# Performance work log

Hardware: AMD Instinct MI355X
Metric: run time of the kernel (lower is better)

The kernel has to match this reference:

```python
import jax, jax.numpy as jnp
import numpy as np

B, T, C, K, V = 4, 4096, 128, 64, 64
EPS = 1e-5


def layer_norm(x, g, b):
    mu = jnp.mean(x, axis=-1, keepdims=True)
    var = jnp.var(x, axis=-1, keepdims=True)
    return (x - mu) * jax.lax.rsqrt(var + EPS) * g + b


def setup_inputs() -> dict:
    key = jax.random.key(0)
    ks = jax.random.split(key, 8)
    s = 1.0 / np.sqrt(C)
    return {
        "x": jax.random.normal(ks[0], (B, T, C), dtype=jnp.float32),
        "Wq": jax.random.uniform(ks[1], (C, K), jnp.float32, -s, s),
        "bq": jnp.zeros((K,), jnp.float32),
        "Wk": jax.random.uniform(ks[2], (C, K), jnp.float32, -s, s),
        "bk": jnp.zeros((K,), jnp.float32),
        "Wv": jax.random.uniform(ks[3], (C, V), jnp.float32, -s, s),
        "bv": jnp.zeros((V,), jnp.float32),
        "gq": jnp.ones((K,), jnp.float32), "bgq": jnp.zeros((K,), jnp.float32),
        "gk": jnp.ones((K,), jnp.float32), "bgk": jnp.zeros((K,), jnp.float32),
        "gv": jnp.ones((V,), jnp.float32), "bgv": jnp.zeros((V,), jnp.float32),
        "go": jnp.ones((V,), jnp.float32), "bgo": jnp.zeros((V,), jnp.float32),
    }


def reference(x, Wq, bq, Wk, bk, Wv, bv, gq, bgq, gk, bgk, gv, bgv, go, bgo):
    # projections: B x T x {K,K,V}
    q = layer_norm(x @ Wq + bq, gq, bgq)
    k = layer_norm(x @ Wk + bk, gk, bgk)
    v = layer_norm(x @ Wv + bv, gv, bgv)
    sqrt_k = jnp.asarray(np.sqrt(K), x.dtype)
    # full B x T x T causal score matrix (faithful to the original bmm+mask)
    logits = jnp.einsum("btk,bsk->bts", q, k) / sqrt_k
    t = jnp.arange(T)
    causal = t[:, None] >= t[None, :]  # lower-triangular incl. diagonal
    logits = jnp.where(causal[None], logits, -jnp.inf)
    probs = jax.nn.softmax(logits, axis=-1)
    read = jnp.einsum("bts,bsv->btv", probs, v)
    read = layer_norm(read, go, bgo)
    return jnp.concatenate([x, read], axis=2)  # B x T x (C+V)
```

## Files before the change

### kernel.cpp

```cpp
#include <hip/hip_runtime.h>

#define TT 4096

typedef unsigned short u16;
typedef unsigned int u32;

typedef short bf16x8 __attribute__((ext_vector_type(8)));
typedef float f32x4 __attribute__((ext_vector_type(4)));

union U8 {
  uint2 q[2];
  uint4 u4;
  bf16x8 v;
  short s[8];
  u32 w[4];
};

static __device__ __forceinline__ u16 f2bf(float f) {
  union { float f; u32 u; } cv;
  cv.f = f;
  u32 r = cv.u + 0x7FFFu + ((cv.u >> 16) & 1u);
  return (u16)(r >> 16);
}
static __device__ __forceinline__ u32 pk2(float a, float b) {
  return (u32)f2bf(a) | ((u32)f2bf(b) << 16);
}
static __device__ __forceinline__ float bf2f(u16 h) {
  union { u32 u; float f; } cv;
  cv.u = ((u32)h) << 16;
  return cv.f;
}
static __device__ __forceinline__ float exp2a(float x) {
  float r; asm("v_exp_f32 %0, %1" : "=v"(r) : "v"(x)); return r;
}
static __device__ __forceinline__ u32 cvtpk(float lo, float hi) {
  u32 r; asm("v_cvt_pk_bf16_f32 %0, %1, %2" : "=v"(r) : "v"(lo), "v"(hi)); return r;
}

__global__ __launch_bounds__(64)
void wpack(const float* __restrict__ Wq, const float* __restrict__ Wk,
           const float* __restrict__ Wv, u16* __restrict__ wf)
{
  const int g = blockIdx.x;
  const int p = g >> 4, s = (g >> 2) & 3, nt = g & 3;
  const int l = threadIdx.x, lg = l >> 4, l15 = l & 15;
  const float* W = (p == 0) ? Wq : (p == 1) ? Wk : Wv;
  const int n = l15 + 16 * nt;
  U8 o;
#pragma unroll
  for (int j = 0; j < 8; ++j) {
    int k = 32 * s + ((j < 4) ? (4 * lg + j) : (16 + 4 * lg + (j - 4)));
    o.s[j] = (short)f2bf(W[k * 64 + n]);
  }
  *(uint4*)(wf + (size_t)(g * 64 + l) * 8) = o.u4;
}

__global__ __launch_bounds__(256)
void proj_mfma(const float* __restrict__ x, const u16* __restrict__ wf,
               const float* __restrict__ bq, const float* __restrict__ bk,
               const float* __restrict__ bv,
               const float* __restrict__ gq, const float* __restrict__ bgq,
               const float* __restrict__ gk, const float* __restrict__ bgk,
               const float* __restrict__ gv, const float* __restrict__ bgv,
               u16* __restrict__ qo, u16* __restrict__ ko, u16* __restrict__ vto,
               float* __restrict__ out)
{
  __shared__ u16 xs[64 * 128];
  const int bx = blockIdx.x;
  const int xcd = bx & 7, i = bx >> 3;
  const int tile = xcd * 32 + (i & 31);
  const int p = i >> 5;
  const int rowbase = tile * 64;
  const int t = threadIdx.x;

  {
    const int row = t >> 2, seg = t & 3;
    const float4* src = (const float4*)(x + (size_t)(rowbase + row) * 128 + seg * 32);
    float4 f[8];
#pragma unroll
    for (int q = 0; q < 8; ++q) f[q] = src[q];
    if ((p == 0 && seg < 2) || (p == 1 && seg >= 2)) {
      float4* dst = (float4*)(out + (size_t)(rowbase + row) * 192 + seg * 32);
#pragma unroll
      for (int q = 0; q < 8; ++q) dst[q] = f[q];
    }
    const int base = row * 256 + seg * 64;
    const int swz = (row & 7) << 4;
    char* xb = (char*)xs;
#pragma unroll
    for (int q = 0; q < 4; ++q) {
      uint4 u;
      u.x = pk2(f[2 * q].x, f[2 * q].y);
      u.y = pk2(f[2 * q].z, f[2 * q].w);
      u.z = pk2(f[2 * q + 1].x, f[2 * q + 1].y);
      u.w = pk2(f[2 * q + 1].z, f[2 * q + 1].w);
      *(uint4*)(xb + ((base + 16 * q) ^ swz)) = u;
    }
  }

  const int w = t >> 6, l = t & 63, lg = l >> 4, l15 = l & 15;
  U8 bfr[4][4];
  const u16* wp = wf + (size_t)p * (16 * 64 * 8);
#pragma unroll
  for (int s = 0; s < 4; ++s)
#pragma unroll
    for (int nt = 0; nt < 4; ++nt)
      bfr[s][nt].u4 = *(const uint4*)(wp + ((s * 4 + nt) * 64 + l) * 8);

  __syncthreads();

  f32x4 acc[4];
#pragma unroll
  for (int nt = 0; nt < 4; ++nt) acc[nt] = (f32x4){0.f, 0.f, 0.f, 0.f};
  const int abase = (16 * w + l15) * 256;
  const int aswz = (l15 & 7) << 4;
  const char* xb = (const char*)xs;
#pragma unroll
  for (int s = 0; s < 4; ++s) {
    U8 af;
    af.q[0] = *(const uint2*)(xb + ((abase + s * 64 + 8 * lg) ^ aswz));
    af.q[1] = *(const uint2*)(xb + ((abase + s * 64 + 8 * lg + 32) ^ aswz));
#pragma unroll
    for (int nt = 0; nt < 4; ++nt)
      acc[nt] = __builtin_amdgcn_mfma_f32_16x16x32_bf16(af.v, bfr[s][nt].v, acc[nt], 0, 0, 0);
  }

  const float* bb = (p == 0) ? bq : (p == 1) ? bk : bv;
  const float* gg = (p == 0) ? gq : (p == 1) ? gk : gv;
  const float* hh = (p == 0) ? bgq : (p == 1) ? bgk : bgv;
  float bcol[4], gcol[4], hcol[4];
#pragma unroll
  for (int nt = 0; nt < 4; ++nt) {
    int col = l15 + 16 * nt;
    bcol[nt] = bb[col]; gcol[nt] = gg[col]; hcol[nt] = hh[col];
  }
  float vals[4][4];
#pragma unroll
  for (int nt = 0; nt < 4; ++nt)
#pragma unroll
    for (int r = 0; r < 4; ++r) vals[nt][r] = acc[nt][r] + bcol[nt];

  float s1[4], s2[4];
#pragma unroll
  for (int r = 0; r < 4; ++r) {
    s1[r] = vals[0][r] + vals[1][r] + vals[2][r] + vals[3][r];
    s2[r] = vals[0][r] * vals[0][r] + vals[1][r] * vals[1][r]
          + vals[2][r] * vals[2][r] + vals[3][r] * vals[3][r];
#pragma unroll
    for (int d = 1; d < 16; d <<= 1) {
      s1[r] += __shfl_xor(s1[r], d);
      s2[r] += __shfl_xor(s2[r], d);
    }
  }

  if (p < 2) {
    u16* dst = (p == 0) ? qo : ko;
#pragma unroll
    for (int r = 0; r < 4; ++r) {
      float mu = s1[r] * (1.f / 64.f);
      float var = s2[r] * (1.f / 64.f) - mu * mu;
      float rs = rsqrtf(var + 1e-5f);
      int grow = rowbase + 16 * w + 4 * lg + r;
#pragma unroll
      for (int nt = 0; nt < 4; ++nt)
        dst[(size_t)grow * 64 + l15 + 16 * nt] =
            f2bf((vals[nt][r] - mu) * rs * gcol[nt] + hcol[nt]);
    }
  } else {
    const int b = rowbase >> 12;
    const int tl0 = (rowbase & 4095) + 16 * w + 4 * lg;
#pragma unroll
    for (int r = 0; r < 4; ++r) {
      float mu = s1[r] * (1.f / 64.f);
      float var = s2[r] * (1.f / 64.f) - mu * mu;
      float rs = rsqrtf(var + 1e-5f);
#pragma unroll
      for (int nt = 0; nt < 4; ++nt)
        vto[(size_t)(b * 64 + l15 + 16 * nt) * TT + tl0 + r] =
            f2bf((vals[nt][r] - mu) * rs * gcol[nt] + hcol[nt]);
    }
  }
}

__global__ __launch_bounds__(256)
void attn_seg4(const u16* __restrict__ qg, const u16* __restrict__ kg,
               const u16* __restrict__ vtg,
               float* __restrict__ mP, float* __restrict__ lP,
               u16* __restrict__ aP)
{
  __shared__ u16 kl4[4 * 64 * 64];
  __shared__ u16 vl4[4 * 64 * 64];
  const int bx = blockIdx.x;
  const int xcd = bx & 7, b = xcd >> 1, e = xcd & 1;
  const int j = e * 272 + (bx >> 3);
  int Q = 0;
  while (2 * (Q + 1) * (Q + 2) <= j) ++Q;
  const int ip = j - 2 * Q * (Q + 1);
  const int dv = ip / (Q + 1);
  const int q = 4 * Q + dv;
  const int s = ip - dv * (Q + 1);
  const int q0 = q * 64;
  const int it0 = s * 4;
  const int it1 = min(it0 + 4, q + 1);

  const int t = threadIdx.x;
  const int w = t >> 6, l = t & 63;
  const int l15 = l & 15, lg = l >> 4;
  const int swzl = (l15 & 7) << 4;

  const int qrow = q0 + 16 * w + l15;
  const u16* qrp = qg + (size_t)(b * TT + qrow) * 64;
  U8 qf[2];
#pragma unroll
  for (int hh = 0; hh < 2; ++hh) {
    qf[hh].q[0] = *(const uint2*)(qrp + 32 * hh + 4 * lg);
    qf[hh].q[1] = *(const uint2*)(qrp + 32 * hh + 4 * lg + 16);
  }

  {
    const int key = t >> 2, part = t & 3;
    const int sbase = key * 128 + part * 32;
    const int ssw = (key & 7) << 4;
    uint4 kr[4][2], vr[4][2];
#pragma unroll
    for (int tt = 0; tt < 4; ++tt) {
      int tile = it0 + tt; if (tile >= it1) tile = it1 - 1;
      const u16* ks = kg + (size_t)(b * TT + tile * 64 + key) * 64 + part * 16;
      kr[tt][0] = ((const uint4*)ks)[0];
      kr[tt][1] = ((const uint4*)ks)[1];
      const u16* vs = vtg + (size_t)(b * 64 + key) * TT + tile * 64 + part * 16;
      vr[tt][0] = ((const uint4*)vs)[0];
      vr[tt][1] = ((const uint4*)vs)[1];
    }
#pragma unroll
    for (int tt = 0; tt < 4; ++tt) {
      char* kd = (char*)kl4 + tt * 8192;
      char* vd = (char*)vl4 + tt * 8192;
      *(uint4*)(kd + ((sbase + 0) ^ ssw)) = kr[tt][0];
      *(uint4*)(kd + ((sbase + 16) ^ ssw)) = kr[tt][1];
      *(uint4*)(vd + ((sbase + 0) ^ ssw)) = vr[tt][0];
      *(uint4*)(vd + ((sbase + 16) ^ ssw)) = vr[tt][1];
    }
  }
  __syncthreads();

  const float C = 0.18033688011112042f;
  float m_run = -1e30f, l_run = 0.f;
  f32x4 acc[4];
#pragma unroll
  for (int ct = 0; ct < 4; ++ct) acc[ct] = (f32x4){0.f, 0.f, 0.f, 0.f};

  int toff = 0;
  for (int it = it0; it < it1; ++it, toff += 8192) {
    const int kb = it * 64;
    const char* kp = (const char*)kl4 + toff;
    const char* vp = (const char*)vl4 + toff;

    f32x4 st[4];
    __builtin_amdgcn_s_setprio(1);
#pragma unroll
    for (int t4 = 0; t4 < 4; ++t4) {
      const int rbase = (16 * t4 + l15) * 128 + 8 * lg;
      U8 kf0, kf1;
      kf0.q[0] = *(const uint2*)(kp + ((rbase + 0) ^ swzl));
      kf0.q[1] = *(const uint2*)(kp + ((rbase + 32) ^ swzl));
      kf1.q[0] = *(const uint2*)(kp + ((rbase + 64) ^ swzl));
      kf1.q[1] = *(const uint2*)(kp + ((rbase + 96) ^ swzl));
      f32x4 d = {0.f, 0.f, 0.f, 0.f};
      d = __builtin_amdgcn_mfma_f32_16x16x32_bf16(kf0.v, qf[0].v, d, 0, 0, 0);
      d = __builtin_amdgcn_mfma_f32_16x16x32_bf16(kf1.v, qf[1].v, d, 0, 0, 0);
      st[t4] = d;
    }
    __builtin_amdgcn_s_setprio(0);

    float sv[16];
    const bool needmask = (kb + 63 > q0 + 16 * w);
    if (needmask) {
#pragma unroll
      for (int t4 = 0; t4 < 4; ++t4) {
#pragma unroll
        for (int r = 0; r < 4; ++r) {
          float sc = st[t4][r] * C;
          int keyidx = kb + 16 * t4 + 4 * lg + r;
          sv[t4 * 4 + r] = (keyidx > qrow) ? -1e30f : sc;
        }
      }
    } else {
#pragma unroll
      for (int t4 = 0; t4 < 4; ++t4) {
#pragma unroll
        for (int r = 0; r < 4; ++r) sv[t4 * 4 + r] = st[t4][r] * C;
      }
    }
    float mx[8];
#pragma unroll
    for (int i = 0; i < 8; ++i) mx[i] = fmaxf(sv[2 * i], sv[2 * i + 1]);
#pragma unroll
    for (int i = 0; i < 4; ++i) mx[i] = fmaxf(mx[2 * i], mx[2 * i + 1]);
    float mt = fmaxf(fmaxf(mx[0], mx[1]), fmaxf(mx[2], mx[3]));
    mt = fmaxf(mt, __shfl_xor(mt, 16));
    mt = fmaxf(mt, __shfl_xor(mt, 32));

    if (!__all(mt - m_run <= 11.5f)) {
      const float mnew = fmaxf(m_run, mt);
      const float al = exp2a(m_run - mnew);
      l_run *= al;
      float ar[4];
#pragma unroll
      for (int r = 0; r < 4; ++r) ar[r] = __shfl(al, 4 * lg + r);
#pragma unroll
      for (int ct = 0; ct < 4; ++ct) {
#pragma unroll
        for (int r = 0; r < 4; ++r) acc[ct][r] *= ar[r];
      }
      m_run = mnew;
    }
    float p[16];
#pragma unroll
    for (int i = 0; i < 16; ++i) p[i] = exp2a(sv[i] - m_run);
    float sm[8];
#pragma unroll
    for (int i = 0; i < 8; ++i) sm[i] = p[2 * i] + p[2 * i + 1];
#pragma unroll
    for (int i = 0; i < 4; ++i) sm[i] = sm[2 * i] + sm[2 * i + 1];
    float rsum = (sm[0] + sm[1]) + (sm[2] + sm[3]);
    rsum += __shfl_xor(rsum, 16);
    rsum += __shfl_xor(rsum, 32);
    l_run += rsum;

    U8 pa[2];
#pragma unroll
    for (int u = 0; u < 2; ++u) {
#pragma unroll
      for (int k2 = 0; k2 < 4; ++k2)
        pa[u].w[k2] = cvtpk(p[8 * u + 2 * k2], p[8 * u + 2 * k2 + 1]);
    }

    __builtin_amdgcn_s_setprio(1);
#pragma unroll
    for (int ct = 0; ct < 4; ++ct) {
      const int vb = (16 * ct + l15) * 128 + 8 * lg;
#pragma unroll
      for (int u = 0; u < 2; ++u) {
        U8 vf;
        vf.q[0] = *(const uint2*)(vp + ((vb + 64 * u + 0) ^ swzl));
        vf.q[1] = *(const uint2*)(vp + ((vb + 64 * u + 32) ^ swzl));
        acc[ct] = __builtin_amdgcn_mfma_f32_16x16x32_bf16(pa[u].v, vf.v, acc[ct], 0, 0, 0);
      }
    }
    __builtin_amdgcn_s_setprio(0);
  }

  const size_t pbase = (size_t)(b * 544 + j) * 64;
  if (lg == 0) {
    mP[pbase + 16 * w + l15] = m_run;
    lP[pbase + 16 * w + l15] = l_run;
  }
#pragma unroll
  for (int ct = 0; ct < 4; ++ct) {
#pragma unroll
    for (int r = 0; r < 4; ++r) {
      int rin = 16 * w + 4 * lg + r;
      aP[(pbase + rin) * 64 + l15 + 16 * ct] = f2bf(acc[ct][r]);
    }
  }
}

__global__ __launch_bounds__(256)
void attn_merge4(const float* __restrict__ mP, const float* __restrict__ lP,
                 const u16* __restrict__ aP,
                 const float* __restrict__ go, const float* __restrict__ bgo,
                 float* __restrict__ out)
{
  const int t = threadIdx.x;
  const int w = t >> 6, c = t & 63;
  const int row = blockIdx.x * 4 + w;
  const int tid2 = row >> 6, rin = row & 63;
  const int b = tid2 >> 6, q = tid2 & 63;
  const int Q = q >> 2;
  const int base_q = b * 544 + 2 * Q * (Q + 1) + (q & 3) * (Q + 1);
  const int ns = Q + 1;

  float m = -1e30f, L = 0.f, o = 0.f;
  for (int s = 0; s < ns; ++s) {
    const size_t pb = (size_t)(base_q + s) * 64;
    float ms = mP[pb + rin];
    float ls = lP[pb + rin];
    float a = bf2f(aP[(pb + rin) * 64 + c]);
    float mn = fmaxf(m, ms);
    float w0 = exp2a(m - mn), w1 = exp2a(ms - mn);
    L = L * w0 + ls * w1;
    o = o * w0 + a * w1;
    m = mn;
  }
  o /= L;

  float s1 = o, s2 = o * o;
#pragma unroll
  for (int d = 1; d < 64; d <<= 1) {
    s1 += __shfl_xor(s1, d);
    s2 += __shfl_xor(s2, d);
  }
  float mu = s1 * (1.f / 64.f);
  float var = s2 * (1.f / 64.f) - mu * mu;
  float rs = rsqrtf(var + 1e-5f);
  out[(size_t)row * 192 + 128 + c] = (o - mu) * rs * go[c] + bgo[c];
}

__global__ __launch_bounds__(256)
void attn_splitW(const u16* __restrict__ qg, const u16* __restrict__ kg,
                 const u16* __restrict__ vtg,
                 float* __restrict__ mP, float* __restrict__ lP,
                 u16* __restrict__ aP,
                 int Wseg, int maxseg, int halfcnt)
{
  __shared__ u16 kl[64 * 64];
  __shared__ u16 vl[64 * 64];
  const int bx = blockIdx.x;
  const int xcd = bx & 7, b = xcd >> 1, e = xcd & 1;
  const int j = e * halfcnt + (bx >> 3);
  const int Wh = Wseg >> 1;
  int Q = 0;
  while (Wh * (Q + 1) * (Q + 2) <= j) ++Q;
  const int ip = j - Wh * Q * (Q + 1);
  const int dv = ip / (Q + 1);
  const int q = Wseg * Q + dv;
  const int s = ip - dv * (Q + 1);
  const int q0 = q * 64;
  const int tileid = b * 64 + q;
  const int it0 = s * Wseg;
  const int it1 = min(it0 + Wseg, q + 1);

  const int t = threadIdx.x;
  const int w = t >> 6, l = t & 63;
  const int l15 = l & 15, lg = l >> 4;
  const int swzl = (l15 & 7) << 4;

  const int qrow = q0 + 16 * w + l15;
  const u16* qrp = qg + (size_t)(b * TT + qrow) * 64;
  U8 qf[2];
#pragma unroll
  for (int hh = 0; hh < 2; ++hh) {
    qf[hh].q[0] = *(const uint2*)(qrp + 32 * hh + 4 * lg);
    qf[hh].q[1] = *(const uint2*)(qrp + 32 * hh + 4 * lg + 16);
  }

  const int key = t >> 2;
  const int part = t & 3;
  const int sbase = key * 128 + part * 32;
  const int ssw = (key & 7) << 4;
  uint4 kr0, kr1, vr0, vr1;
  {
    const u16* ks = kg + (size_t)(b * TT + it0 * 64 + key) * 64 + part * 16;
    kr0 = ((const uint4*)ks)[0];
    kr1 = ((const uint4*)ks)[1];
    const u16* vs = vtg + (size_t)(b * 64 + key) * TT + it0 * 64 + part * 16;
    vr0 = ((const uint4*)vs)[0];
    vr1 = ((const uint4*)vs)[1];
  }

  float m_run = -1e30f, l_run = 0.f;
  f32x4 acc[4];
#pragma unroll
  for (int ct = 0; ct < 4; ++ct) acc[ct] = (f32x4){0.f, 0.f, 0.f, 0.f};

  for (int it = it0; it < it1; ++it) {
    const int kb = it * 64;
    {
      char* kd = (char*)kl;
      char* vd = (char*)vl;
      *(uint4*)(kd + ((sbase + 0) ^ ssw)) = kr0;
      *(uint4*)(kd + ((sbase + 16) ^ ssw)) = kr1;
      *(uint4*)(vd + ((sbase + 0) ^ ssw)) = vr0;
      *(uint4*)(vd + ((sbase + 16) ^ ssw)) = vr1;
    }
    __syncthreads();
    if (it + 1 < it1) {
      const u16* ks = kg + (size_t)(b * TT + (it + 1) * 64 + key) * 64 + part * 16;
      kr0 = ((const uint4*)ks)[0];
      kr1 = ((const uint4*)ks)[1];
      const u16* vs = vtg + (size_t)(b * 64 + key) * TT + (it + 1) * 64 + part * 16;
      vr0 = ((const uint4*)vs)[0];
      vr1 = ((const uint4*)vs)[1];
    }

    f32x4 st[4];
#pragma unroll
    for (int t4 = 0; t4 < 4; ++t4) {
      const int rbase = (16 * t4 + l15) * 128 + 8 * lg;
      const char* kp = (const char*)kl;
      U8 kf0, kf1;
      kf0.q[0] = *(const uint2*)(kp + ((rbase + 0) ^ swzl));
      kf0.q[1] = *(const uint2*)(kp + ((rbase + 32) ^ swzl));
      kf1.q[0] = *(const uint2*)(kp + ((rbase + 64) ^ swzl));
      kf1.q[1] = *(const uint2*)(kp + ((rbase + 96) ^ swzl));
      f32x4 d = {0.f, 0.f, 0.f, 0.f};
      d = __builtin_amdgcn_mfma_f32_16x16x32_bf16(kf0.v, qf[0].v, d, 0, 0, 0);
      d = __builtin_amdgcn_mfma_f32_16x16x32_bf16(kf1.v, qf[1].v, d, 0, 0, 0);
      st[t4] = d;
    }

    float sv[16];
    const bool needmask = (kb + 63 > q0 + 16 * w);
#pragma unroll
    for (int t4 = 0; t4 < 4; ++t4) {
#pragma unroll
      for (int r = 0; r < 4; ++r) {
        float sc = st[t4][r] * 0.125f;
        if (needmask) {
          int keyidx = kb + 16 * t4 + 4 * lg + r;
          if (keyidx > qrow) sc = -1e30f;
        }
        sv[t4 * 4 + r] = sc;
      }
    }
    float mt = sv[0];
#pragma unroll
    for (int i = 1; i < 16; ++i) mt = fmaxf(mt, sv[i]);
    mt = fmaxf(mt, __shfl_xor(mt, 16));
    mt = fmaxf(mt, __shfl_xor(mt, 32));
    const float mnew = fmaxf(m_run, mt);
    const float al = __expf(m_run - mnew);
    float pv[16];
    float rsum = 0.f;
#pragma unroll
    for (int i = 0; i < 16; ++i) { pv[i] = __expf(sv[i] - mnew); rsum += pv[i]; }
    rsum += __shfl_xor(rsum, 16);
    rsum += __shfl_xor(rsum, 32);
    l_run = l_run * al + rsum;
    m_run = mnew;
    float ar[4];
#pragma unroll
    for (int r = 0; r < 4; ++r) ar[r] = __shfl(al, 4 * lg + r);
#pragma unroll
    for (int ct = 0; ct < 4; ++ct) {
#pragma unroll
      for (int r = 0; r < 4; ++r) acc[ct][r] *= ar[r];
    }
    U8 pa[2];
#pragma unroll
    for (int u = 0; u < 2; ++u) {
#pragma unroll
      for (int i = 0; i < 8; ++i) pa[u].s[i] = (short)f2bf(pv[8 * u + i]);
    }

#pragma unroll
    for (int ct = 0; ct < 4; ++ct) {
      const int vb = (16 * ct + l15) * 128 + 8 * lg;
      const char* vp = (const char*)vl;
#pragma unroll
      for (int u = 0; u < 2; ++u) {
        U8 vf;
        vf.q[0] = *(const uint2*)(vp + ((vb + 64 * u + 0) ^ swzl));
        vf.q[1] = *(const uint2*)(vp + ((vb + 64 * u + 32) ^ swzl));
        acc[ct] = __builtin_amdgcn_mfma_f32_16x16x32_bf16(pa[u].v, vf.v, acc[ct], 0, 0, 0);
      }
    }
    __syncthreads();
  }

  const size_t pbase = (size_t)(tileid * maxseg + s) * 64;
  if (lg == 0) {
    mP[pbase + 16 * w + l15] = m_run;
    lP[pbase + 16 * w + l15] = l_run;
  }
#pragma unroll
  for (int ct = 0; ct < 4; ++ct) {
#pragma unroll
    for (int r = 0; r < 4; ++r) {
      int rin = 16 * w + 4 * lg + r;
      aP[(pbase + rin) * 64 + l15 + 16 * ct] = f2bf(acc[ct][r]);
    }
  }
}

__global__ __launch_bounds__(256)
void attn_mergeW(const float* __restrict__ mP, const float* __restrict__ lP,
                 const u16* __restrict__ aP,
                 const float* __restrict__ go, const float* __restrict__ bgo,
                 float* __restrict__ out, int jshift, int maxseg)
{
  const int t = threadIdx.x;
  const int w = t >> 6, c = t & 63;
  const int row = blockIdx.x * 4 + w;
  const int tid2 = row >> 6, rin = row & 63;
  const int q = tid2 & 63;
  const int ns = (q >> jshift) + 1;

  float m = -1e30f, L = 0.f, o = 0.f;
  for (int s = 0; s < ns; ++s) {
    const size_t pbase = (size_t)(tid2 * maxseg + s) * 64;
    float ms = mP[pbase + rin];
    float ls = lP[pbase + rin];
    float a = bf2f(aP[(pbase + rin) * 64 + c]);
    float mn = fmaxf(m, ms);
    float w0 = __expf(m - mn), w1 = __expf(ms - mn);
    L = L * w0 + ls * w1;
    o = o * w0 + a * w1;
    m = mn;
  }
  o /= L;

  float s1 = o, s2 = o * o;
#pragma unroll
  for (int d = 1; d < 64; d <<= 1) {
    s1 += __shfl_xor(s1, d);
    s2 += __shfl_xor(s2, d);
  }
  float mu = s1 * (1.f / 64.f);
  float var = s2 * (1.f / 64.f) - mu * mu;
  float rs = rsqrtf(var + 1e-5f);
  out[(size_t)row * 192 + 128 + c] = (o - mu) * rs * go[c] + bgo[c];
}

__global__ __launch_bounds__(128)
void attn1(const u16* __restrict__ qg, const u16* __restrict__ kg,
           const u16* __restrict__ vtg,
           const float* __restrict__ go, const float* __restrict__ bgo,
           float* __restrict__ out)
{
  __shared__ u16 kl[64 * 64];
  __shared__ u16 vl[64 * 64];
  const int bx = blockIdx.x;
  const int tt = (bx < 256) ? bx : (767 - bx);
  const int b = tt >> 7;
  const int q0 = (tt & 127) * 32;
  const int tid = threadIdx.x;
  const int w = tid >> 6;
  const int l = tid & 63;
  const int l15 = l & 15;
  const int lg = l >> 4;
  const int swzl = (l15 & 7) << 4;

  const int qrow = q0 + 16 * w + l15;
  const u16* qrp = qg + (size_t)(b * TT + qrow) * 64;
  U8 qf[2];
#pragma unroll
  for (int h = 0; h < 2; ++h) {
    qf[h].q[0] = *(const uint2*)(qrp + 32 * h + 4 * lg);
    qf[h].q[1] = *(const uint2*)(qrp + 32 * h + 4 * lg + 16);
  }

  float m_run = -1e30f, l_run = 0.f;
  f32x4 acc[4];
#pragma unroll
  for (int ct = 0; ct < 4; ++ct) acc[ct] = (f32x4){0.f, 0.f, 0.f, 0.f};

  const int nkv = (q0 >> 6) + 1;
  for (int it = 0; it < nkv; ++it) {
    const int kb = it * 64;
    {
      const int key = tid >> 1;
      const int dh = (tid & 1) * 32;
      const u16* ks = kg + (size_t)(b * TT + kb + key) * 64 + dh;
      uint4 d0 = *(const uint4*)(ks + 0);
      uint4 d1 = *(const uint4*)(ks + 8);
      uint4 d2 = *(const uint4*)(ks + 16);
      uint4 d3 = *(const uint4*)(ks + 24);
      const int base = key * 128 + dh * 2;
      const int sw = (key & 7) << 4;
      char* kd = (char*)kl;
      *(uint4*)(kd + ((base + 0) ^ sw)) = d0;
      *(uint4*)(kd + ((base + 16) ^ sw)) = d1;
      *(uint4*)(kd + ((base + 32) ^ sw)) = d2;
      *(uint4*)(kd + ((base + 48) ^ sw)) = d3;
      const u16* vs = vtg + (size_t)(b * 64 + key) * TT + kb + dh;
      uint4 e0 = *(const uint4*)(vs + 0);
      uint4 e1 = *(const uint4*)(vs + 8);
      uint4 e2 = *(const uint4*)(vs + 16);
      uint4 e3 = *(const uint4*)(vs + 24);
      char* vd = (char*)vl;
      *(uint4*)(vd + ((base + 0) ^ sw)) = e0;
      *(uint4*)(vd + ((base + 16) ^ sw)) = e1;
      *(uint4*)(vd + ((base + 32) ^ sw)) = e2;
      *(uint4*)(vd + ((base + 48) ^ sw)) = e3;
    }
    __syncthreads();

    f32x4 st[4];
#pragma unroll
    for (int t4 = 0; t4 < 4; ++t4) {
      const int rbase = (16 * t4 + l15) * 128 + 8 * lg;
      const char* kp = (const char*)kl;
      U8 kf0, kf1;
      kf0.q[0] = *(const uint2*)(kp + ((rbase + 0) ^ swzl));
      kf0.q[1] = *(const uint2*)(kp + ((rbase + 32) ^ swzl));
      kf1.q[0] = *(const uint2*)(kp + ((rbase + 64) ^ swzl));
      kf1.q[1] = *(const uint2*)(kp + ((rbase + 96) ^ swzl));
      f32x4 d = {0.f, 0.f, 0.f, 0.f};
      d = __builtin_amdgcn_mfma_f32_16x16x32_bf16(kf0.v, qf[0].v, d, 0, 0, 0);
      d = __builtin_amdgcn_mfma_f32_16x16x32_bf16(kf1.v, qf[1].v, d, 0, 0, 0);
      st[t4] = d;
    }

    float sv[16];
    const bool needmask = (kb + 63 > q0 + 16 * w);
#pragma unroll
    for (int t4 = 0; t4 < 4; ++t4) {
#pragma unroll
      for (int r = 0; r < 4; ++r) {
        float sc = st[t4][r] * 0.125f;
        if (needmask) {
          int keyidx = kb + 16 * t4 + 4 * lg + r;
          if (keyidx > qrow) sc = -1e30f;
        }
        sv[t4 * 4 + r] = sc;
      }
    }
    float mt = sv[0];
#pragma unroll
    for (int i = 1; i < 16; ++i) mt = fmaxf(mt, sv[i]);
    mt = fmaxf(mt, __shfl_xor(mt, 16));
    mt = fmaxf(mt, __shfl_xor(mt, 32));
    const float mnew = fmaxf(m_run, mt);
    const float al = __expf(m_run - mnew);
    float p[16];
    float rsum = 0.f;
#pragma unroll
    for (int i = 0; i < 16; ++i) { p[i] = __expf(sv[i] - mnew); rsum += p[i]; }
    rsum += __shfl_xor(rsum, 16);
    rsum += __shfl_xor(rsum, 32);
    l_run = l_run * al + rsum;
    m_run = mnew;
    float ar[4];
#pragma unroll
    for (int r = 0; r < 4; ++r) ar[r] = __shfl(al, 4 * lg + r);
#pragma unroll
    for (int ct = 0; ct < 4; ++ct) {
#pragma unroll
      for (int r = 0; r < 4; ++r) acc[ct][r] *= ar[r];
    }
    U8 pa[2];
#pragma unroll
    for (int u = 0; u < 2; ++u) {
#pragma unroll
      for (int i = 0; i < 8; ++i) pa[u].s[i] = (short)f2bf(p[8 * u + i]);
    }

#pragma unroll
    for (int ct = 0; ct < 4; ++ct) {
      const int vb = (16 * ct + l15) * 128 + 8 * lg;
      const char* vp = (const char*)vl;
#pragma unroll
      for (int u = 0; u < 2; ++u) {
        U8 vf;
        vf.q[0] = *(const uint2*)(vp + ((vb + 64 * u + 0) ^ swzl));
        vf.q[1] = *(const uint2*)(vp + ((vb + 64 * u + 32) ^ swzl));
        acc[ct] = __builtin_amdgcn_mfma_f32_16x16x32_bf16(pa[u].v, vf.v, acc[ct], 0, 0, 0);
      }
    }
    __syncthreads();
  }

  float linv[4];
#pragma unroll
  for (int r = 0; r < 4; ++r) linv[r] = 1.f / __shfl(l_run, 4 * lg + r);
  float o[4][4];
#pragma unroll
  for (int ct = 0; ct < 4; ++ct) {
#pragma unroll
    for (int r = 0; r < 4; ++r) o[ct][r] = acc[ct][r] * linv[r];
  }
  float s1[4], s2[4];
#pragma unroll
  for (int r = 0; r < 4; ++r) {
    s1[r] = o[0][r] + o[1][r] + o[2][r] + o[3][r];
    s2[r] = o[0][r] * o[0][r] + o[1][r] * o[1][r] + o[2][r] * o[2][r] + o[3][r] * o[3][r];
#pragma unroll
    for (int d = 1; d < 16; d <<= 1) {
      s1[r] += __shfl_xor(s1[r], d);
      s2[r] += __shfl_xor(s2[r], d);
    }
  }
  float gov[4], bgv2[4];
#pragma unroll
  for (int ct = 0; ct < 4; ++ct) {
    gov[ct] = go[16 * ct + l15];
    bgv2[ct] = bgo[16 * ct + l15];
  }
#pragma unroll
  for (int r = 0; r < 4; ++r) {
    float mu = s1[r] * (1.f / 64.f);
    float var = s2[r] * (1.f / 64.f) - mu * mu;
    float rs = rsqrtf(var + 1e-5f);
    int row = q0 + 16 * w + 4 * lg + r;
    float* op = out + (size_t)(b * TT + row) * 192 + 128;
#pragma unroll
    for (int ct = 0; ct < 4; ++ct)
      op[16 * ct + l15] = (o[ct][r] - mu) * rs * gov[ct] + bgv2[ct];
  }
}

extern "C" void kernel_launch(void* const* d_in, const int* in_sizes, int n_in,
                              void* d_out, int out_size, void* d_ws, size_t ws_size,
                              hipStream_t stream) {
  (void)in_sizes; (void)n_in; (void)out_size;
  const float* x   = (const float*)d_in[0];
  const float* Wq  = (const float*)d_in[1];
  const float* bq  = (const float*)d_in[2];
  const float* Wk  = (const float*)d_in[3];
  const float* bk  = (const float*)d_in[4];
  const float* Wv  = (const float*)d_in[5];
  const float* bv  = (const float*)d_in[6];
  const float* gq  = (const float*)d_in[7];
  const float* bgq = (const float*)d_in[8];
  const float* gk  = (const float*)d_in[9];
  const float* bgk = (const float*)d_in[10];
  const float* gv  = (const float*)d_in[11];
  const float* bgv = (const float*)d_in[12];
  const float* go  = (const float*)d_in[13];
  const float* bgo = (const float*)d_in[14];
  float* out = (float*)d_out;

  char* wsb = (char*)d_ws;
  u16* qws  = (u16*)wsb;
  u16* kws  = (u16*)(wsb + (2u << 20));
  u16* vtws = (u16*)(wsb + (4u << 20));
  u16* wfr  = (u16*)(wsb + (6u << 20));
  const size_t OFF_MP = (6u << 20) + 65536;

  wpack<<<48, 64, 0, stream>>>(Wq, Wk, Wv, wfr);
  proj_mfma<<<768, 256, 0, stream>>>(x, wfr, bq, bk, bv,
                                     gq, bgq, gk, bgk, gv, bgv,
                                     qws, kws, vtws, out);

  {
    const size_t SEG4 = 4u * 544;
    const size_t MPS4 = SEG4 * 64 * 4;
    const size_t APS4 = SEG4 * 64 * 64 * 2;
    const size_t OFF_LP4 = OFF_MP + MPS4;
    const size_t OFF_AP4 = OFF_LP4 + MPS4;
    const size_t NEED4 = OFF_AP4 + APS4;
    const size_t MPS8 = 256u * 8 * 64 * 4;
    const size_t APS8 = 256u * 8 * 64 * 64 * 2;
    const size_t OFF_LP8 = OFF_MP + MPS8;
    const size_t OFF_AP8 = OFF_LP8 + MPS8;
    const size_t NEED8 = OFF_AP8 + APS8;
    const size_t MPS32 = 256u * 2 * 64 * 4;
    const size_t APS32 = 256u * 2 * 64 * 64 * 2;
    const size_t OFF_LP32 = OFF_MP + MPS32;
    const size_t OFF_AP32 = OFF_LP32 + MPS32;
    const size_t NEED32 = OFF_AP32 + APS32;

    if (ws_size >= NEED4) {
      float* mP = (float*)(wsb + OFF_MP);
      float* lP = (float*)(wsb + OFF_LP4);
      u16*   aP = (u16*)(wsb + OFF_AP4);
      attn_seg4<<<2176, 256, 0, stream>>>(qws, kws, vtws, mP, lP, aP);
      attn_merge4<<<4096, 256, 0, stream>>>(mP, lP, aP, go, bgo, out);
    } else if (ws_size >= NEED8) {
      float* mP = (float*)(wsb + OFF_MP);
      float* lP = (float*)(wsb + OFF_LP8);
      u16*   aP = (u16*)(wsb + OFF_AP8);
      attn_splitW<<<1152, 256, 0, stream>>>(qws, kws, vtws, mP, lP, aP, 8, 8, 144);
      attn_mergeW<<<4096, 256, 0, stream>>>(mP, lP, aP, go, bgo, out, 3, 8);
    } else if (ws_size >= NEED32) {
      float* mP = (float*)(wsb + OFF_MP);
      float* lP = (float*)(wsb + OFF_LP32);
      u16*   aP = (u16*)(wsb + OFF_AP32);
      attn_splitW<<<384, 256, 0, stream>>>(qws, kws, vtws, mP, lP, aP, 32, 2, 48);
      attn_mergeW<<<4096, 256, 0, stream>>>(mP, lP, aP, go, bgo, out, 5, 2);
    } else {
      attn1<<<512, 128, 0, stream>>>(qws, kws, vtws, go, bgo, out);
    }
  }
}
```

Baseline: 65.21 us.

## Pair adjacent query tiles per block to reuse staged K/V, and transpose V through LDS

Result: slower. 94.11 us (+44.3%).

```diff
diff --git a/kernel.cpp b/kernel.cpp
--- a/kernel.cpp
+++ b/kernel.cpp
@@ -35,6 +35,73 @@
 }
 static __device__ __forceinline__ u32 cvtpk(float lo, float hi) {
   u32 r; asm("v_cvt_pk_bf16_f32 %0, %1, %2" : "=v"(r) : "v"(lo), "v"(hi)); return r;
+}
+
+static __device__ __forceinline__ void sm_step(
+    const f32x4* st, int kb, int wbase, int qrow, int lg,
+    float& m_run, float& l_run, f32x4* acc, U8* pa)
+{
+  const float C = 0.18033688011112042f;
+  float sv[16];
+  const bool needmask = (kb + 63 > wbase);
+  if (needmask) {
+#pragma unroll
+    for (int t4 = 0; t4 < 4; ++t4) {
+#pragma unroll
+      for (int r = 0; r < 4; ++r) {
+        float sc = st[t4][r] * C;
+        int keyidx = kb + 16 * t4 + 4 * lg + r;
+        sv[t4 * 4 + r] = (keyidx > qrow) ? -1e30f : sc;
+      }
+    }
+  } else {
+#pragma unroll
+    for (int t4 = 0; t4 < 4; ++t4) {
+#pragma unroll
+      for (int r = 0; r < 4; ++r) sv[t4 * 4 + r] = st[t4][r] * C;
+    }
+  }
+  float mx[8];
+#pragma unroll
+  for (int i = 0; i < 8; ++i) mx[i] = fmaxf(sv[2 * i], sv[2 * i + 1]);
+#pragma unroll
+  for (int i = 0; i < 4; ++i) mx[i] = fmaxf(mx[2 * i], mx[2 * i + 1]);
+  float mt = fmaxf(fmaxf(mx[0], mx[1]), fmaxf(mx[2], mx[3]));
+  mt = fmaxf(mt, __shfl_xor(mt, 16));
+  mt = fmaxf(mt, __shfl_xor(mt, 32));
+
+  if (!__all(mt - m_run <= 11.5f)) {
+    const float mnew = fmaxf(m_run, mt);
+    const float al = exp2a(m_run - mnew);
+    l_run *= al;
+    float ar[4];
+#pragma unroll
+    for (int r = 0; r < 4; ++r) ar[r] = __shfl(al, 4 * lg + r);
+#pragma unroll
+    for (int ct = 0; ct < 4; ++ct) {
+#pragma unroll
+      for (int r = 0; r < 4; ++r) acc[ct][r] *= ar[r];
+    }
+    m_run = mnew;
+  }
+  float p[16];
+#pragma unroll
+  for (int i = 0; i < 16; ++i) p[i] = exp2a(sv[i] - m_run);
+  float sm[8];
+#pragma unroll
+  for (int i = 0; i < 8; ++i) sm[i] = p[2 * i] + p[2 * i + 1];
+#pragma unroll
+  for (int i = 0; i < 4; ++i) sm[i] = sm[2 * i] + sm[2 * i + 1];
+  float rsum = (sm[0] + sm[1]) + (sm[2] + sm[3]);
+  rsum += __shfl_xor(rsum, 16);
+  rsum += __shfl_xor(rsum, 32);
+  l_run += rsum;
+#pragma unroll
+  for (int u = 0; u < 2; ++u) {
+#pragma unroll
+    for (int k2 = 0; k2 < 4; ++k2)
+      pa[u].w[k2] = cvtpk(p[8 * u + 2 * k2], p[8 * u + 2 * k2 + 1]);
+  }
 }
 
 __global__ __launch_bounds__(64)
@@ -65,7 +132,7 @@
                u16* __restrict__ qo, u16* __restrict__ ko, u16* __restrict__ vto,
                float* __restrict__ out)
 {
-  __shared__ u16 xs[64 * 128];
+  __shared__ u16 xs[64 * 130];
   const int bx = blockIdx.x;
   const int xcd = bx & 7, i = bx >> 3;
   const int tile = xcd * 32 + (i & 31);
@@ -167,54 +234,72 @@
             f2bf((vals[nt][r] - mu) * rs * gcol[nt] + hcol[nt]);
     }
   } else {
-    const int b = rowbase >> 12;
-    const int tl0 = (rowbase & 4095) + 16 * w + 4 * lg;
+    u16* vls = xs;
+    __syncthreads();
 #pragma unroll
     for (int r = 0; r < 4; ++r) {
       float mu = s1[r] * (1.f / 64.f);
       float var = s2[r] * (1.f / 64.f) - mu * mu;
       float rs = rsqrtf(var + 1e-5f);
+      int row = 16 * w + 4 * lg + r;
 #pragma unroll
       for (int nt = 0; nt < 4; ++nt)
-        vto[(size_t)(b * 64 + l15 + 16 * nt) * TT + tl0 + r] =
+        vls[row * 65 + l15 + 16 * nt] =
             f2bf((vals[nt][r] - mu) * rs * gcol[nt] + hcol[nt]);
     }
+    __syncthreads();
+    const int b = rowbase >> 12;
+    const int tl = rowbase & 4095;
+    const int col = t >> 2;
+    const int tq = (t & 3) * 16;
+    U8 o0, o1;
+#pragma unroll
+    for (int i = 0; i < 8; ++i) o0.s[i] = (short)vls[(tq + i) * 65 + col];
+#pragma unroll
+    for (int i = 0; i < 8; ++i) o1.s[i] = (short)vls[(tq + 8 + i) * 65 + col];
+    u16* dst = vto + (size_t)(b * 64 + col) * TT + tl + tq;
+    *(uint4*)(dst + 0) = o0.u4;
+    *(uint4*)(dst + 8) = o1.u4;
   }
 }
 
 __global__ __launch_bounds__(256)
-void attn_seg4(const u16* __restrict__ qg, const u16* __restrict__ kg,
-               const u16* __restrict__ vtg,
-               float* __restrict__ mP, float* __restrict__ lP,
-               u16* __restrict__ aP)
+void attn_pair4(const u16* __restrict__ qg, const u16* __restrict__ kg,
+                const u16* __restrict__ vtg,
+                float* __restrict__ mP, float* __restrict__ lP,
+                u16* __restrict__ aP)
 {
   __shared__ u16 kl4[4 * 64 * 64];
   __shared__ u16 vl4[4 * 64 * 64];
   const int bx = blockIdx.x;
-  const int xcd = bx & 7, b = xcd >> 1, e = xcd & 1;
-  const int j = e * 272 + (bx >> 3);
-  int Q = 0;
-  while (2 * (Q + 1) * (Q + 2) <= j) ++Q;
-  const int ip = j - 2 * Q * (Q + 1);
-  const int dv = ip / (Q + 1);
-  const int q = 4 * Q + dv;
-  const int s = ip - dv * (Q + 1);
-  const int q0 = q * 64;
-  const int it0 = s * 4;
-  const int it1 = min(it0 + 4, q + 1);
+  const int xcd = bx & 7, b = xcd >> 1, e2 = xcd & 1;
+  const int j = e2 * 136 + (bx >> 3);
+  int M = 0;
+  while ((M + 1) * (M + 2) <= j) ++M;
+  const int ip = j - M * (M + 1);
+  const int e = (ip >= M + 1) ? 1 : 0;
+  const int s = ip - e * (M + 1);
+  const int pr = 2 * M + e;
+  const int qa = 2 * pr, qb = 2 * pr + 1;
+  const int it0 = 4 * s;
+  const int it1 = min(it0 + 4, qb + 1);
 
   const int t = threadIdx.x;
   const int w = t >> 6, l = t & 63;
   const int l15 = l & 15, lg = l >> 4;
   const int swzl = (l15 & 7) << 4;
 
-  const int qrow = q0 + 16 * w + l15;
-  const u16* qrp = qg + (size_t)(b * TT + qrow) * 64;
-  U8 qf[2];
+  const int wbaseA = qa * 64 + 16 * w, wbaseB = qb * 64 + 16 * w;
+  const int qrowA = wbaseA + l15, qrowB = wbaseB + l15;
+  const u16* qrpA = qg + (size_t)(b * TT + qrowA) * 64;
+  const u16* qrpB = qg + (size_t)(b * TT + qrowB) * 64;
+  U8 qfA[2], qfB[2];
 #pragma unroll
   for (int hh = 0; hh < 2; ++hh) {
-    qf[hh].q[0] = *(const uint2*)(qrp + 32 * hh + 4 * lg);
-    qf[hh].q[1] = *(const uint2*)(qrp + 32 * hh + 4 * lg + 16);
+    qfA[hh].q[0] = *(const uint2*)(qrpA + 32 * hh + 4 * lg);
+    qfA[hh].q[1] = *(const uint2*)(qrpA + 32 * hh + 4 * lg + 16);
+    qfB[hh].q[0] = *(const uint2*)(qrpB + 32 * hh + 4 * lg);
+    qfB[hh].q[1] = *(const uint2*)(qrpB + 32 * hh + 4 * lg + 16);
   }
 
   {
@@ -244,19 +329,22 @@
   }
   __syncthreads();
 
-  const float C = 0.18033688011112042f;
-  float m_run = -1e30f, l_run = 0.f;
-  f32x4 acc[4];
-#pragma unroll
-  for (int ct = 0; ct < 4; ++ct) acc[ct] = (f32x4){0.f, 0.f, 0.f, 0.f};
+  float mA = -1e30f, lA = 0.f, mB = -1e30f, lB = 0.f;
+  f32x4 accA[4], accB[4];
+#pragma unroll
+  for (int ct = 0; ct < 4; ++ct) {
+    accA[ct] = (f32x4){0.f, 0.f, 0.f, 0.f};
+    accB[ct] = (f32x4){0.f, 0.f, 0.f, 0.f};
+  }
 
   int toff = 0;
   for (int it = it0; it < it1; ++it, toff += 8192) {
     const int kb = it * 64;
     const char* kp = (const char*)kl4 + toff;
     const char* vp = (const char*)vl4 + toff;
-
-    f32x4 st[4];
+    const bool liveA = (it <= qa);
+
+    f32x4 stA[4], stB[4];
     __builtin_amdgcn_s_setprio(1);
 #pragma unroll
     for (int t4 = 0; t4 < 4; ++t4) {
@@ -266,75 +354,22 @@
       kf0.q[1] = *(const uint2*)(kp + ((rbase + 32) ^ swzl));
       kf1.q[0] = *(const uint2*)(kp + ((rbase + 64) ^ swzl));
       kf1.q[1] = *(const uint2*)(kp + ((rbase + 96) ^ swzl));
-      f32x4 d = {0.f, 0.f, 0.f, 0.f};
-      d = __builtin_amdgcn_mfma_f32_16x16x32_bf16(kf0.v, qf[0].v, d, 0, 0, 0);
-      d = __builtin_amdgcn_mfma_f32_16x16x32_bf16(kf1.v, qf[1].v, d, 0, 0, 0);
-      st[t4] = d;
+      if (liveA) {
+        f32x4 d = {0.f, 0.f, 0.f, 0.f};
+        d = __builtin_amdgcn_mfma_f32_16x16x32_bf16(kf0.v, qfA[0].v, d, 0, 0, 0);
+        d = __builtin_amdgcn_mfma_f32_16x16x32_bf16(kf1.v, qfA[1].v, d, 0, 0, 0);
+        stA[t4] = d;
+      }
+      f32x4 db = {0.f, 0.f, 0.f, 0.f};
+      db = __builtin_amdgcn_mfma_f32_16x16x32_bf16(kf0.v, qfB[0].v, db, 0, 0, 0);
+      db = __builtin_amdgcn_mfma_f32_16x16x32_bf16(kf1.v, qfB[1].v, db, 0, 0, 0);
+      stB[t4] = db;
     }
     __builtin_amdgcn_s_setprio(0);
 
-    float sv[16];
-    const bool needmask = (kb + 63 > q0 + 16 * w);
-    if (needmask) {
-#pragma unroll
-      for (int t4 = 0; t4 < 4; ++t4) {
-#pragma unroll
-        for (int r = 0; r < 4; ++r) {
-          float sc = st[t4][r] * C;
-          int keyidx = kb + 16 * t4 + 4 * lg + r;
-          sv[t4 * 4 + r] = (keyidx > qrow) ? -1e30f : sc;
-        }
-      }
-    } else {
-#pragma unroll
-      for (int t4 = 0; t4 < 4; ++t4) {
-#pragma unroll
-        for (int r = 0; r < 4; ++r) sv[t4 * 4 + r] = st[t4][r] * C;
-      }
-    }
-    float mx[8];
-#pragma unroll
-    for (int i = 0; i < 8; ++i) mx[i] = fmaxf(sv[2 * i], sv[2 * i + 1]);
-#pragma unroll
-    for (int i = 0; i < 4; ++i) mx[i] = fmaxf(mx[2 * i], mx[2 * i + 1]);
-    float mt = fmaxf(fmaxf(mx[0], mx[1]), fmaxf(mx[2], mx[3]));
-    mt = fmaxf(mt, __shfl_xor(mt, 16));
-    mt = fmaxf(mt, __shfl_xor(mt, 32));
-
-    if (!__all(mt - m_run <= 11.5f)) {
-      const float mnew = fmaxf(m_run, mt);
-      const float al = exp2a(m_run - mnew);
-      l_run *= al;
-      float ar[4];
-#pragma unroll
-      for (int r = 0; r < 4; ++r) ar[r] = __shfl(al, 4 * lg + r);
-#pragma unroll
-      for (int ct = 0; ct < 4; ++ct) {
-#pragma unroll
-        for (int r = 0; r < 4; ++r) acc[ct][r] *= ar[r];
-      }
-      m_run = mnew;
-    }
-    float p[16];
-#pragma unroll
-    for (int i = 0; i < 16; ++i) p[i] = exp2a(sv[i] - m_run);
-    float sm[8];
-#pragma unroll
-    for (int i = 0; i < 8; ++i) sm[i] = p[2 * i] + p[2 * i + 1];
-#pragma unroll
-    for (int i = 0; i < 4; ++i) sm[i] = sm[2 * i] + sm[2 * i + 1];
-    float rsum = (sm[0] + sm[1]) + (sm[2] + sm[3]);
-    rsum += __shfl_xor(rsum, 16);
-    rsum += __shfl_xor(rsum, 32);
-    l_run += rsum;
-
-    U8 pa[2];
-#pragma unroll
-    for (int u = 0; u < 2; ++u) {
-#pragma unroll
-      for (int k2 = 0; k2 < 4; ++k2)
-        pa[u].w[k2] = cvtpk(p[8 * u + 2 * k2], p[8 * u + 2 * k2 + 1]);
-    }
+    U8 paA[2], paB[2];
+    if (liveA) sm_step(stA, kb, wbaseA, qrowA, lg, mA, lA, accA, paA);
+    sm_step(stB, kb, wbaseB, qrowB, lg, mB, lB, accB, paB);
 
     __builtin_amdgcn_s_setprio(1);
 #pragma unroll
@@ -345,23 +380,32 @@
         U8 vf;
         vf.q[0] = *(const uint2*)(vp + ((vb + 64 * u + 0) ^ swzl));
         vf.q[1] = *(const uint2*)(vp + ((vb + 64 * u + 32) ^ swzl));
-        acc[ct] = __builtin_amdgcn_mfma_f32_16x16x32_bf16(pa[u].v, vf.v, acc[ct], 0, 0, 0);
+        if (liveA)
+          accA[ct] = __builtin_amdgcn_mfma_f32_16x16x32_bf16(paA[u].v, vf.v, accA[ct], 0, 0, 0);
+        accB[ct] = __builtin_amdgcn_mfma_f32_16x16x32_bf16(paB[u].v, vf.v, accB[ct], 0, 0, 0);
       }
     }
     __builtin_amdgcn_s_setprio(0);
   }
 
-  const size_t pbase = (size_t)(b * 544 + j) * 64;
+  const int QA = qa >> 2, QB = qb >> 2;
+  const int jqA = 2 * QA * (QA + 1) + (qa & 3) * (QA + 1) + s;
+  const int jqB = 2 * QB * (QB + 1) + (qb & 3) * (QB + 1) + s;
+  const size_t pbA = (size_t)(b * 544 + jqA) * 64;
+  const size_t pbB = (size_t)(b * 544 + jqB) * 64;
   if (lg == 0) {
-    mP[pbase + 16 * w + l15] = m_run;
-    lP[pbase + 16 * w + l15] = l_run;
+    mP[pbA + 16 * w + l15] = mA;
+    lP[pbA + 16 * w + l15] = lA;
+    mP[pbB + 16 * w + l15] = mB;
+    lP[pbB + 16 * w + l15] = lB;
   }
 #pragma unroll
   for (int ct = 0; ct < 4; ++ct) {
 #pragma unroll
     for (int r = 0; r < 4; ++r) {
       int rin = 16 * w + 4 * lg + r;
-      aP[(pbase + rin) * 64 + l15 + 16 * ct] = f2bf(acc[ct][r]);
+      aP[(pbA + rin) * 64 + l15 + 16 * ct] = f2bf(accA[ct][r]);
+      aP[(pbB + rin) * 64 + l15 + 16 * ct] = f2bf(accB[ct][r]);
     }
   }
 }
@@ -846,7 +890,7 @@
       float* mP = (float*)(wsb + OFF_MP);
       float* lP = (float*)(wsb + OFF_LP4);
       u16*   aP = (u16*)(wsb + OFF_AP4);
-      attn_seg4<<<2176, 256, 0, stream>>>(qws, kws, vtws, mP, lP, aP);
+      attn_pair4<<<1088, 256, 0, stream>>>(qws, kws, vtws, mP, lP, aP);
       attn_merge4<<<4096, 256, 0, stream>>>(mP, lP, aP, go, bgo, out);
     } else if (ws_size >= NEED8) {
       float* mP = (float*)(wsb + OFF_MP);
```
